# Performance work log

Measured on AMD Instinct MI355X. Metric: run time of the kernel, lower is better.

## Reference

```python
import jax, jax.numpy as jnp
import numpy as np

N_NODES = 100000
N_EDGES = 1600000
DIM = 64
L = 5
NUM_GRAPHS = 256
BN_EPS = 1e-5


def setup_inputs() -> dict:
    key = jax.random.key(0)
    ks = jax.random.split(key, 8)
    x = jax.random.normal(ks[0], (N_NODES, DIM), dtype=jnp.float32)
    edge_index = jax.random.randint(ks[1], (2, N_EDGES), 0, N_NODES, dtype=jnp.int32).astype(jnp.int64)
    batch = jnp.sort(jax.random.randint(ks[2], (N_NODES,), 0, NUM_GRAPHS, dtype=jnp.int32)).astype(jnp.int64)
    W1 = jax.random.normal(ks[3], (L, DIM, DIM), dtype=jnp.float32) * (1.0 / np.sqrt(DIM))
    b1 = jnp.zeros((L, DIM), dtype=jnp.float32)
    W2 = jax.random.normal(ks[4], (L, DIM, DIM), dtype=jnp.float32) * (1.0 / np.sqrt(DIM))
    b2 = jnp.zeros((L, DIM), dtype=jnp.float32)
    gamma = jnp.ones((L, DIM), dtype=jnp.float32)
    beta = jnp.zeros((L, DIM), dtype=jnp.float32)
    return {"x": x, "edge_index": edge_index, "batch": batch, "W1": W1, "b1": b1, "W2": W2, "b2": b2, "gamma": gamma, "beta": beta}


def reference(x, edge_index, batch, W1, b1, W2, b2, gamma, beta):
    src, dst = edge_index[0], edge_index[1]
    n = x.shape[0]
    h = x
    xs = []
    for i in range(L):
        # GINConv (eps=0): h_i' = MLP(h_i + sum_{j->i} h_j), scatter-add over edges
        agg = jax.ops.segment_sum(h[src], dst, num_segments=n)
        z = h + agg
        z = jnp.maximum(z @ W1[i] + b1[i], 0.0) @ W2[i] + b2[i]
        z = jnp.maximum(z, 0.0)  # outer ReLU
        # BatchNorm1d, training-mode batch stats (biased var)
        mu = jnp.mean(z, axis=0)
        var = jnp.mean((z - mu) ** 2, axis=0)
        z = (z - mu) * jax.lax.rsqrt(var + BN_EPS) * gamma[i] + beta[i]
        xs.append(z)
        h = z
    counts = jax.ops.segment_sum(jnp.ones((n,), dtype=x.dtype), batch, num_segments=NUM_GRAPHS)
    counts = jnp.maximum(counts, 1.0)[:, None]
    xpool = [jax.ops.segment_sum(z, batch, num_segments=NUM_GRAPHS) / counts for z in xs]
    return jnp.concatenate(xpool, axis=1), jnp.concatenate(xs, axis=1)
```

## Files before the change

kernel.cpp:

```cpp
#include <hip/hip_runtime.h>

#define N_NODES 100000
#define N_EDGES 1600000
#define DIM 64
#define NLAYERS 5
#define NUM_GRAPHS 256
#define BN_EPS 1e-5f
#define STATS_BLOCKS 256
#define CSR_CAP 32
#define OV_CAP 65536
#define NSHARD 4
#define SHARD_W (N_NODES / NSHARD)
#define NBLK ((N_NODES + 255) / 256)

typedef _Float16 f16;
typedef _Float16 f16x4 __attribute__((ext_vector_type(4)));

__global__ __launch_bounds__(256) void build_csr_shard_kernel(
        const int* __restrict__ ei, int* __restrict__ cursor,
        int* __restrict__ csr, int* __restrict__ ovcnt, int* __restrict__ ovpairs,
        int lo, int hi) {
    int e = blockIdx.x * 256 + threadIdx.x;
    if (e >= N_EDGES) return;
    int t = ei[N_EDGES + e];
    if (t < lo || t >= hi) return;
    int s = ei[e];
    int c = atomicAdd(&cursor[t], 1);
    if (c < CSR_CAP) {
        csr[t * CSR_CAP + c] = s;
    } else {
        int o = atomicAdd(ovcnt, 1);
        if (o < OV_CAP) { ovpairs[2 * o] = t; ovpairs[2 * o + 1] = s; }
    }
}

__global__ void cast_x_kernel(const float* __restrict__ x, f16* __restrict__ h16) {
    long t = (long)blockIdx.x * 256 + threadIdx.x;
    if (t >= (long)N_NODES * DIM / 4) return;
    float4 v = ((const float4*)x)[t];
    f16x4 p = { (f16)v.x, (f16)v.y, (f16)v.z, (f16)v.w };
    *(f16x4*)(h16 + t * 4) = p;
}

__global__ __launch_bounds__(256) void aggregate_f16_kernel(
        const int* __restrict__ csr, const int* __restrict__ deg,
        const int* __restrict__ ovcnt, const int* __restrict__ ovpairs,
        const f16* __restrict__ h16, const float* __restrict__ hself, int hstride,
        float* __restrict__ agg) {
    long tid = (long)blockIdx.x * 256 + threadIdx.x;
    int n = (int)(tid >> 6);
    int d = (int)(tid & 63);
    if (n >= N_NODES) return;
    int dval = deg[n];
    int cnt = min(dval, CSR_CAP);
    const int4* row = (const int4*)(csr + n * CSR_CAP);
    float own = hself[(long)n * hstride + d];
    float a0 = 0.f, a1 = 0.f, a2 = 0.f, a3 = 0.f;
    float a4 = 0.f, a5 = 0.f, a6 = 0.f, a7 = 0.f;
    for (int k = 0; k < cnt; k += 8) {
        int4 ra = row[k >> 2];
        int4 rb = row[(k >> 2) + 1];
        int s0 = (k + 0 < cnt) ? ra.x : 0;
        int s1 = (k + 1 < cnt) ? ra.y : 0;
        int s2 = (k + 2 < cnt) ? ra.z : 0;
        int s3 = (k + 3 < cnt) ? ra.w : 0;
        int s4 = (k + 4 < cnt) ? rb.x : 0;
        int s5 = (k + 5 < cnt) ? rb.y : 0;
        int s6 = (k + 6 < cnt) ? rb.z : 0;
        int s7 = (k + 7 < cnt) ? rb.w : 0;
        float v0 = (float)h16[(long)s0 * DIM + d];
        float v1 = (float)h16[(long)s1 * DIM + d];
        float v2 = (float)h16[(long)s2 * DIM + d];
        float v3 = (float)h16[(long)s3 * DIM + d];
        float v4 = (float)h16[(long)s4 * DIM + d];
        float v5 = (float)h16[(long)s5 * DIM + d];
        float v6 = (float)h16[(long)s6 * DIM + d];
        float v7 = (float)h16[(long)s7 * DIM + d];
        a0 += (k + 0 < cnt) ? v0 : 0.f;
        a1 += (k + 1 < cnt) ? v1 : 0.f;
        a2 += (k + 2 < cnt) ? v2 : 0.f;
        a3 += (k + 3 < cnt) ? v3 : 0.f;
        a4 += (k + 4 < cnt) ? v4 : 0.f;
        a5 += (k + 5 < cnt) ? v5 : 0.f;
        a6 += (k + 6 < cnt) ? v6 : 0.f;
        a7 += (k + 7 < cnt) ? v7 : 0.f;
    }
    if (dval > CSR_CAP) {
        int m = min(*ovcnt, OV_CAP);
        for (int i = 0; i < m; ++i) {
            if (ovpairs[2 * i] == n) a0 += (float)h16[(long)ovpairs[2 * i + 1] * DIM + d];
        }
    }
    agg[(long)n * DIM + d] = own + ((a0 + a1) + (a2 + a3)) + ((a4 + a5) + (a6 + a7));
}

__global__ __launch_bounds__(256) void mlp_gemm_kernel(
        const float* __restrict__ in, const float* __restrict__ W,
        const float* __restrict__ b, float* __restrict__ out) {
    __shared__ __align__(16) float sW[DIM * DIM];
    __shared__ float sb[DIM];
    for (int k = threadIdx.x; k < DIM * DIM / 4; k += 256)
        ((float4*)sW)[k] = ((const float4*)W)[k];
    if (threadIdx.x < DIM) sb[threadIdx.x] = b[threadIdx.x];
    __syncthreads();

    int p = threadIdx.x & 127;
    int j0 = (threadIdx.x >> 7) * 32;
    int base = blockIdx.x * 256;
    int n0 = base + p;
    int n1 = base + 128 + p;
    bool v1 = n1 < N_NODES;
    const float* inr0 = in + (long)n0 * DIM;
    const float* inr1 = in + (long)(v1 ? n1 : n0) * DIM;

    float acc0[32], acc1[32];
#pragma unroll
    for (int j = 0; j < 32; ++j) { acc0[j] = sb[j0 + j]; acc1[j] = acc0[j]; }

    for (int d4 = 0; d4 < DIM / 4; ++d4) {
        float4 za = ((const float4*)inr0)[d4];
        float4 zb = ((const float4*)inr1)[d4];
        const float* w0 = sW + (d4 * 4 + 0) * DIM + j0;
        const float* w1 = sW + (d4 * 4 + 1) * DIM + j0;
        const float* w2 = sW + (d4 * 4 + 2) * DIM + j0;
        const float* w3 = sW + (d4 * 4 + 3) * DIM + j0;
#pragma unroll
        for (int j = 0; j < 32; j += 4) {
            float4 a0 = *(const float4*)(w0 + j);
            float4 a1 = *(const float4*)(w1 + j);
            float4 a2 = *(const float4*)(w2 + j);
            float4 a3 = *(const float4*)(w3 + j);
            acc0[j + 0] += za.x * a0.x + za.y * a1.x + za.z * a2.x + za.w * a3.x;
            acc0[j + 1] += za.x * a0.y + za.y * a1.y + za.z * a2.y + za.w * a3.y;
            acc0[j + 2] += za.x * a0.z + za.y * a1.z + za.z * a2.z + za.w * a3.z;
            acc0[j + 3] += za.x * a0.w + za.y * a1.w + za.z * a2.w + za.w * a3.w;
            acc1[j + 0] += zb.x * a0.x + zb.y * a1.x + zb.z * a2.x + zb.w * a3.x;
            acc1[j + 1] += zb.x * a0.y + zb.y * a1.y + zb.z * a2.y + zb.w * a3.y;
            acc1[j + 2] += zb.x * a0.z + zb.y * a1.z + zb.z * a2.z + zb.w * a3.z;
            acc1[j + 3] += zb.x * a0.w + zb.y * a1.w + zb.z * a2.w + zb.w * a3.w;
        }
    }

    float* o0 = out + (long)n0 * DIM + j0;
#pragma unroll
    for (int j = 0; j < 32; j += 4) {
        float4 v = { fmaxf(acc0[j], 0.f), fmaxf(acc0[j + 1], 0.f),
                     fmaxf(acc0[j + 2], 0.f), fmaxf(acc0[j + 3], 0.f) };
        *(float4*)(o0 + j) = v;
    }
    if (v1) {
        float* o1 = out + (long)n1 * DIM + j0;
#pragma unroll
        for (int j = 0; j < 32; j += 4) {
            float4 v = { fmaxf(acc1[j], 0.f), fmaxf(acc1[j + 1], 0.f),
                         fmaxf(acc1[j + 2], 0.f), fmaxf(acc1[j + 3], 0.f) };
            *(float4*)(o1 + j) = v;
        }
    }
}

__global__ void stats_partial_kernel(const float* __restrict__ z, float* __restrict__ partials) {
    __shared__ float red[2 * 256];
    int d = threadIdx.x & 63;
    int slot = threadIdx.x >> 6;
    const int S = STATS_BLOCKS * 4;
    float s1 = 0.f, s2 = 0.f;
    int n = blockIdx.x * 4 + slot;
    for (; n + 3 * S < N_NODES; n += 4 * S) {
        float v0 = z[(long)(n + 0 * S) * DIM + d];
        float v1 = z[(long)(n + 1 * S) * DIM + d];
        float v2 = z[(long)(n + 2 * S) * DIM + d];
        float v3 = z[(long)(n + 3 * S) * DIM + d];
        s1 += v0 + v1 + v2 + v3;
        s2 += v0 * v0 + v1 * v1 + v2 * v2 + v3 * v3;
    }
    for (; n < N_NODES; n += S) {
        float v = z[(long)n * DIM + d];
        s1 += v;
        s2 += v * v;
    }
    red[threadIdx.x] = s1;
    red[256 + threadIdx.x] = s2;
    __syncthreads();
    if (threadIdx.x < 64) {
        float a = red[d] + red[64 + d] + red[128 + d] + red[192 + d];
        float c = red[256 + d] + red[320 + d] + red[384 + d] + red[448 + d];
        partials[blockIdx.x * 128 + d] = a;
        partials[blockIdx.x * 128 + 64 + d] = c;
    }
}

__global__ void stats_finalize_kernel(const float* __restrict__ partials,
                                      const float* __restrict__ gamma,
                                      const float* __restrict__ beta,
                                      float* __restrict__ ss) {
    __shared__ float r1[256], r2[256];
    int d = threadIdx.x & 63, q = threadIdx.x >> 6;
    float s1 = 0.f, s2 = 0.f;
    for (int b2_ = q; b2_ < STATS_BLOCKS; b2_ += 4) {
        s1 += partials[b2_ * 128 + d];
        s2 += partials[b2_ * 128 + 64 + d];
    }
    r1[threadIdx.x] = s1;
    r2[threadIdx.x] = s2;
    __syncthreads();
    if (threadIdx.x < 64) {
        s1 = r1[d] + r1[64 + d] + r1[128 + d] + r1[192 + d];
        s2 = r2[d] + r2[64 + d] + r2[128 + d] + r2[192 + d];
        float mu = s1 * (1.f / N_NODES);
        float var = s2 * (1.f / N_NODES) - mu * mu;
        float rs = 1.f / sqrtf(fmaxf(var, 0.f) + BN_EPS);
        float sc = gamma[d] * rs;
        ss[d] = sc;
        ss[64 + d] = beta[d] - mu * sc;
    }
}

__global__ void bn_apply_kernel(const float* __restrict__ z, const float* __restrict__ ss,
                                float* __restrict__ outxs, f16* __restrict__ h16) {
    long t = (long)blockIdx.x * 256 + threadIdx.x;
    if (t >= (long)N_NODES * (DIM / 4)) return;
    int r = (int)(t & 15);
    long n = t >> 4;
    float4 v = ((const float4*)(z + n * DIM))[r];
    float4 sc = ((const float4*)ss)[r];
    float4 sh = ((const float4*)(ss + DIM))[r];
    float4 o = { v.x * sc.x + sh.x, v.y * sc.y + sh.y,
                 v.z * sc.z + sh.z, v.w * sc.w + sh.w };
    ((float4*)(outxs + n * (DIM * NLAYERS)))[r] = o;
    if (h16) {
        f16x4 p = { (f16)o.x, (f16)o.y, (f16)o.z, (f16)o.w };
        *(f16x4*)(h16 + n * DIM + r * 4) = p;
    }
}

__global__ void graph_starts_kernel(const int* __restrict__ batch, int* __restrict__ starts) {
    int g = threadIdx.x;
    if (g > NUM_GRAPHS) return;
    int lo = 0, hi = N_NODES;
    while (lo < hi) {
        int mid = (lo + hi) >> 1;
        if (batch[mid] < g) lo = mid + 1; else hi = mid;
    }
    starts[g] = lo;
}

__global__ __launch_bounds__(64) void pool_kernel(
        const float* __restrict__ xs, const int* __restrict__ starts,
        float* __restrict__ outpool) {
    int g = blockIdx.x;
    int d = blockIdx.y * 64 + threadIdx.x;
    int s = starts[g], e = starts[g + 1];
    const int LD = DIM * NLAYERS;
    float a0 = 0.f, a1 = 0.f, a2 = 0.f, a3 = 0.f;
    float a4 = 0.f, a5 = 0.f, a6 = 0.f, a7 = 0.f;
    int n = s;
    for (; n + 8 <= e; n += 8) {
        a0 += xs[(long)(n + 0) * LD + d];
        a1 += xs[(long)(n + 1) * LD + d];
        a2 += xs[(long)(n + 2) * LD + d];
        a3 += xs[(long)(n + 3) * LD + d];
        a4 += xs[(long)(n + 4) * LD + d];
        a5 += xs[(long)(n + 5) * LD + d];
        a6 += xs[(long)(n + 6) * LD + d];
        a7 += xs[(long)(n + 7) * LD + d];
    }
    for (; n < e; ++n) a0 += xs[(long)n * LD + d];
    float acc = ((a0 + a1) + (a2 + a3)) + ((a4 + a5) + (a6 + a7));
    outpool[(long)g * LD + d] = acc / fmaxf((float)(e - s), 1.f);
}

static inline size_t rup(size_t x) { return (x + 255) & ~(size_t)255; }

extern "C" void kernel_launch(void* const* d_in, const int* in_sizes, int n_in,
                              void* d_out, int out_size, void* d_ws, size_t ws_size,
                              hipStream_t stream) {
    const float* x     = (const float*)d_in[0];
    const int*   ei    = (const int*)d_in[1];
    const int*   batch = (const int*)d_in[2];
    const float* W1    = (const float*)d_in[3];
    const float* b1    = (const float*)d_in[4];
    const float* W2    = (const float*)d_in[5];
    const float* b2    = (const float*)d_in[6];
    const float* gamma = (const float*)d_in[7];
    const float* beta  = (const float*)d_in[8];

    float* out      = (float*)d_out;
    float* out_pool = out;
    float* out_xs   = out + (size_t)NUM_GRAPHS * DIM * NLAYERS;

    char* w = (char*)d_ws;
    int*   csr      = (int*)w;    w += rup((size_t)N_NODES * CSR_CAP * 4);
    int*   cursor   = (int*)w;    w += rup((size_t)N_NODES * 4);
    int*   ovcnt    = (int*)w;    w += 256;
    int*   ovpairs  = (int*)w;    w += rup((size_t)OV_CAP * 8);
    float* agg      = (float*)w;  w += rup((size_t)N_NODES * DIM * 4);
    float* bufB     = (float*)w;  w += rup((size_t)N_NODES * DIM * 4);
    f16*   h16      = (f16*)w;    w += rup((size_t)N_NODES * DIM * 2);
    float* partials = (float*)w;  w += rup((size_t)STATS_BLOCKS * 128 * 4);
    float* ss       = (float*)w;  w += 512;
    int*   starts   = (int*)w;    w += rup((size_t)(NUM_GRAPHS + 1) * 4);
    float* zbuf     = agg;

    hipMemsetAsync(cursor, 0, (size_t)N_NODES * 4, stream);
    hipMemsetAsync(ovcnt, 0, 4, stream);
    for (int sh = 0; sh < NSHARD; ++sh) {
        build_csr_shard_kernel<<<(N_EDGES + 255) / 256, 256, 0, stream>>>(
            ei, cursor, csr, ovcnt, ovpairs, sh * SHARD_W, (sh + 1) * SHARD_W);
    }
    cast_x_kernel<<<((long)N_NODES * DIM / 4 + 255) / 256, 256, 0, stream>>>(x, h16);
    graph_starts_kernel<<<1, 320, 0, stream>>>(batch, starts);

    const float* hself = x;
    int hs = DIM;
    for (int l = 0; l < NLAYERS; ++l) {
        aggregate_f16_kernel<<<((long)N_NODES * DIM + 255) / 256, 256, 0, stream>>>(
            csr, cursor, ovcnt, ovpairs, h16, hself, hs, agg);
        mlp_gemm_kernel<<<NBLK, 256, 0, stream>>>(
            agg, W1 + (size_t)l * DIM * DIM, b1 + (size_t)l * DIM, bufB);
        mlp_gemm_kernel<<<NBLK, 256, 0, stream>>>(
            bufB, W2 + (size_t)l * DIM * DIM, b2 + (size_t)l * DIM, zbuf);
        stats_partial_kernel<<<STATS_BLOCKS, 256, 0, stream>>>(zbuf, partials);
        stats_finalize_kernel<<<1, 256, 0, stream>>>(partials, gamma + (size_t)l * DIM,
                                                     beta + (size_t)l * DIM, ss);
        bn_apply_kernel<<<((long)N_NODES * (DIM / 4) + 255) / 256, 256, 0, stream>>>(
            zbuf, ss, out_xs + (size_t)l * DIM, (l + 1 < NLAYERS) ? h16 : nullptr);
        hself = out_xs + (size_t)l * DIM;
        hs = DIM * NLAYERS;
    }

    pool_kernel<<<dim3(NUM_GRAPHS, NLAYERS), 64, 0, stream>>>(out_xs, starts, out_pool);
}
```

Baseline: 863.1 us.

## Vectorize aggregation to half2 per lane and fuse BN stats finalize via last-block

The aggregation kernel now gives each half-wavefront one node, and each lane loads two fp16 features (f16x2) per neighbor. This halves the number of gather instructions and widens the stores to float2. The separate stats finalize launch is folded into the partial-stats kernel using a last-block-done atomic counter stored next to ovcnt. This saves one launch per layer but adds a threadfence and an atomic handshake.

```diff
diff --git a/kernel.cpp b/kernel.cpp
--- a/kernel.cpp
+++ b/kernel.cpp
@@ -14,6 +14,7 @@
 #define NBLK ((N_NODES + 255) / 256)
 
 typedef _Float16 f16;
+typedef _Float16 f16x2 __attribute__((ext_vector_type(2)));
 typedef _Float16 f16x4 __attribute__((ext_vector_type(4)));
 
 __global__ __launch_bounds__(256) void build_csr_shard_kernel(
@@ -47,19 +48,24 @@
         const int* __restrict__ ovcnt, const int* __restrict__ ovpairs,
         const f16* __restrict__ h16, const float* __restrict__ hself, int hstride,
         float* __restrict__ agg) {
-    long tid = (long)blockIdx.x * 256 + threadIdx.x;
-    int n = (int)(tid >> 6);
-    int d = (int)(tid & 63);
-    if (n >= N_NODES) return;
+    int lane = threadIdx.x & 63;
+    int half = lane >> 5;
+    int ll = lane & 31;
+    int n = blockIdx.x * 8 + (threadIdx.x >> 6) * 2 + half;
+
     int dval = deg[n];
     int cnt = min(dval, CSR_CAP);
-    const int4* row = (const int4*)(csr + n * CSR_CAP);
-    float own = hself[(long)n * hstride + d];
-    float a0 = 0.f, a1 = 0.f, a2 = 0.f, a3 = 0.f;
-    float a4 = 0.f, a5 = 0.f, a6 = 0.f, a7 = 0.f;
+    const int4* row4 = (const int4*)(csr + n * CSR_CAP);
+
+    float2 own = *(const float2*)(hself + (long)n * hstride + 2 * ll);
+    float ax0 = own.x, ay0 = own.y;
+    float ax1 = 0.f, ay1 = 0.f, ax2 = 0.f, ay2 = 0.f, ax3 = 0.f, ay3 = 0.f;
+    float ax4 = 0.f, ay4 = 0.f, ax5 = 0.f, ay5 = 0.f, ax6 = 0.f, ay6 = 0.f;
+    float ax7 = 0.f, ay7 = 0.f;
+
     for (int k = 0; k < cnt; k += 8) {
-        int4 ra = row[k >> 2];
-        int4 rb = row[(k >> 2) + 1];
+        int4 ra = row4[k >> 2];
+        int4 rb = row4[(k >> 2) + 1];
         int s0 = (k + 0 < cnt) ? ra.x : 0;
         int s1 = (k + 1 < cnt) ? ra.y : 0;
         int s2 = (k + 2 < cnt) ? ra.z : 0;
@@ -68,30 +74,35 @@
         int s5 = (k + 5 < cnt) ? rb.y : 0;
         int s6 = (k + 6 < cnt) ? rb.z : 0;
         int s7 = (k + 7 < cnt) ? rb.w : 0;
-        float v0 = (float)h16[(long)s0 * DIM + d];
-        float v1 = (float)h16[(long)s1 * DIM + d];
-        float v2 = (float)h16[(long)s2 * DIM + d];
-        float v3 = (float)h16[(long)s3 * DIM + d];
-        float v4 = (float)h16[(long)s4 * DIM + d];
-        float v5 = (float)h16[(long)s5 * DIM + d];
-        float v6 = (float)h16[(long)s6 * DIM + d];
-        float v7 = (float)h16[(long)s7 * DIM + d];
-        a0 += (k + 0 < cnt) ? v0 : 0.f;
-        a1 += (k + 1 < cnt) ? v1 : 0.f;
-        a2 += (k + 2 < cnt) ? v2 : 0.f;
-        a3 += (k + 3 < cnt) ? v3 : 0.f;
-        a4 += (k + 4 < cnt) ? v4 : 0.f;
-        a5 += (k + 5 < cnt) ? v5 : 0.f;
-        a6 += (k + 6 < cnt) ? v6 : 0.f;
-        a7 += (k + 7 < cnt) ? v7 : 0.f;
+        f16x2 v0 = *(const f16x2*)(h16 + (long)s0 * DIM + 2 * ll);
+        f16x2 v1 = *(const f16x2*)(h16 + (long)s1 * DIM + 2 * ll);
+        f16x2 v2 = *(const f16x2*)(h16 + (long)s2 * DIM + 2 * ll);
+        f16x2 v3 = *(const f16x2*)(h16 + (long)s3 * DIM + 2 * ll);
+        f16x2 v4 = *(const f16x2*)(h16 + (long)s4 * DIM + 2 * ll);
+        f16x2 v5 = *(const f16x2*)(h16 + (long)s5 * DIM + 2 * ll);
+        f16x2 v6 = *(const f16x2*)(h16 + (long)s6 * DIM + 2 * ll);
+        f16x2 v7 = *(const f16x2*)(h16 + (long)s7 * DIM + 2 * ll);
+        if (k + 0 < cnt) { ax0 += (float)v0.x; ay0 += (float)v0.y; }
+        if (k + 1 < cnt) { ax1 += (float)v1.x; ay1 += (float)v1.y; }
+        if (k + 2 < cnt) { ax2 += (float)v2.x; ay2 += (float)v2.y; }
+        if (k + 3 < cnt) { ax3 += (float)v3.x; ay3 += (float)v3.y; }
+        if (k + 4 < cnt) { ax4 += (float)v4.x; ay4 += (float)v4.y; }
+        if (k + 5 < cnt) { ax5 += (float)v5.x; ay5 += (float)v5.y; }
+        if (k + 6 < cnt) { ax6 += (float)v6.x; ay6 += (float)v6.y; }
+        if (k + 7 < cnt) { ax7 += (float)v7.x; ay7 += (float)v7.y; }
     }
     if (dval > CSR_CAP) {
         int m = min(*ovcnt, OV_CAP);
         for (int i = 0; i < m; ++i) {
-            if (ovpairs[2 * i] == n) a0 += (float)h16[(long)ovpairs[2 * i + 1] * DIM + d];
+            if (ovpairs[2 * i] == n) {
+                f16x2 v = *(const f16x2*)(h16 + (long)ovpairs[2 * i + 1] * DIM + 2 * ll);
+                ax0 += (float)v.x; ay0 += (float)v.y;
+            }
         }
     }
-    agg[(long)n * DIM + d] = own + ((a0 + a1) + (a2 + a3)) + ((a4 + a5) + (a6 + a7));
+    float2 o = { ((ax0 + ax1) + (ax2 + ax3)) + ((ax4 + ax5) + (ax6 + ax7)),
+                 ((ay0 + ay1) + (ay2 + ay3)) + ((ay4 + ay5) + (ay6 + ay7)) };
+    *(float2*)(agg + (long)n * DIM + 2 * ll) = o;
 }
 
 __global__ __launch_bounds__(256) void mlp_gemm_kernel(
@@ -159,8 +170,13 @@
     }
 }
 
-__global__ void stats_partial_kernel(const float* __restrict__ z, float* __restrict__ partials) {
+__global__ void stats_kernel(const float* __restrict__ z,
+                             const float* __restrict__ gamma,
+                             const float* __restrict__ beta,
+                             float* __restrict__ partials, float* __restrict__ ss,
+                             int* __restrict__ done) {
     __shared__ float red[2 * 256];
+    __shared__ int lastflag;
     int d = threadIdx.x & 63;
     int slot = threadIdx.x >> 6;
     const int S = STATS_BLOCKS * 4;
@@ -188,32 +204,37 @@
         partials[blockIdx.x * 128 + d] = a;
         partials[blockIdx.x * 128 + 64 + d] = c;
     }
-}
-
-__global__ void stats_finalize_kernel(const float* __restrict__ partials,
-                                      const float* __restrict__ gamma,
-                                      const float* __restrict__ beta,
-                                      float* __restrict__ ss) {
-    __shared__ float r1[256], r2[256];
-    int d = threadIdx.x & 63, q = threadIdx.x >> 6;
-    float s1 = 0.f, s2 = 0.f;
-    for (int b2_ = q; b2_ < STATS_BLOCKS; b2_ += 4) {
-        s1 += partials[b2_ * 128 + d];
-        s2 += partials[b2_ * 128 + 64 + d];
-    }
-    r1[threadIdx.x] = s1;
-    r2[threadIdx.x] = s2;
+    __threadfence();
+    __syncthreads();
+    if (threadIdx.x == 0)
+        lastflag = (atomicAdd(done, 1) == STATS_BLOCKS - 1);
+    __syncthreads();
+    if (!lastflag) return;
+
+    int q = threadIdx.x >> 6;
+    float t1 = 0.f, t2 = 0.f;
+    for (int b = q; b < STATS_BLOCKS; b += 4) {
+        t1 += __hip_atomic_load(&partials[b * 128 + d], __ATOMIC_RELAXED,
+                                __HIP_MEMORY_SCOPE_AGENT);
+        t2 += __hip_atomic_load(&partials[b * 128 + 64 + d], __ATOMIC_RELAXED,
+                                __HIP_MEMORY_SCOPE_AGENT);
+    }
+    __syncthreads();
+    red[threadIdx.x] = t1;
+    red[256 + threadIdx.x] = t2;
     __syncthreads();
     if (threadIdx.x < 64) {
-        s1 = r1[d] + r1[64 + d] + r1[128 + d] + r1[192 + d];
-        s2 = r2[d] + r2[64 + d] + r2[128 + d] + r2[192 + d];
-        float mu = s1 * (1.f / N_NODES);
-        float var = s2 * (1.f / N_NODES) - mu * mu;
+        t1 = red[d] + red[64 + d] + red[128 + d] + red[192 + d];
+        t2 = red[256 + d] + red[320 + d] + red[384 + d] + red[448 + d];
+        float mu = t1 * (1.f / N_NODES);
+        float var = t2 * (1.f / N_NODES) - mu * mu;
         float rs = 1.f / sqrtf(fmaxf(var, 0.f) + BN_EPS);
         float sc = gamma[d] * rs;
         ss[d] = sc;
         ss[64 + d] = beta[d] - mu * sc;
     }
+    if (threadIdx.x == 0)
+        __hip_atomic_store(done, 0, __ATOMIC_RELAXED, __HIP_MEMORY_SCOPE_AGENT);
 }
 
 __global__ void bn_apply_kernel(const float* __restrict__ z, const float* __restrict__ ss,
@@ -303,7 +324,7 @@
     float* zbuf     = agg;
 
     hipMemsetAsync(cursor, 0, (size_t)N_NODES * 4, stream);
-    hipMemsetAsync(ovcnt, 0, 4, stream);
+    hipMemsetAsync(ovcnt, 0, 8, stream);
     for (int sh = 0; sh < NSHARD; ++sh) {
         build_csr_shard_kernel<<<(N_EDGES + 255) / 256, 256, 0, stream>>>(
             ei, cursor, csr, ovcnt, ovpairs, sh * SHARD_W, (sh + 1) * SHARD_W);
@@ -314,15 +335,15 @@
     const float* hself = x;
     int hs = DIM;
     for (int l = 0; l < NLAYERS; ++l) {
-        aggregate_f16_kernel<<<((long)N_NODES * DIM + 255) / 256, 256, 0, stream>>>(
+        aggregate_f16_kernel<<<N_NODES / 8, 256, 0, stream>>>(
             csr, cursor, ovcnt, ovpairs, h16, hself, hs, agg);
         mlp_gemm_kernel<<<NBLK, 256, 0, stream>>>(
             agg, W1 + (size_t)l * DIM * DIM, b1 + (size_t)l * DIM, bufB);
         mlp_gemm_kernel<<<NBLK, 256, 0, stream>>>(
             bufB, W2 + (size_t)l * DIM * DIM, b2 + (size_t)l * DIM, zbuf);
-        stats_partial_kernel<<<STATS_BLOCKS, 256, 0, stream>>>(zbuf, partials);
-        stats_finalize_kernel<<<1, 256, 0, stream>>>(partials, gamma + (size_t)l * DIM,
-                                                     beta + (size_t)l * DIM, ss);
+        stats_kernel<<<STATS_BLOCKS, 256, 0, stream>>>(
+            zbuf, gamma + (size_t)l * DIM, beta + (size_t)l * DIM,
+            partials, ss, ovcnt + 1);
         bn_apply_kernel<<<((long)N_NODES * (DIM / 4) + 255) / 256, 256, 0, stream>>>(
             zbuf, ss, out_xs + (size_t)l * DIM, (l + 1 < NLAYERS) ? h16 : nullptr);
         hself = out_xs + (size_t)l * DIM;
```

Result: slower. 906.6 us (+5.0%).

## Retile MLP GEMM to four rows per thread and fuse BN stats finalize

Applied to the files above, without the earlier changes.

The MLP GEMM now has each thread compute 4 node rows by 16 output columns instead of 2 rows by 32 columns. Each weight value read from shared memory is therefore reused across more rows. Separately, the BN statistics finalize step moves into the partial-stats kernel using a last-block-done atomic counter, which removes one kernel launch per layer. The counter lives next to the overflow count and relies on __threadfence plus relaxed atomic loads for correctness.

```diff
diff --git a/kernel.cpp b/kernel.cpp
--- a/kernel.cpp
+++ b/kernel.cpp
@@ -104,63 +104,79 @@
     if (threadIdx.x < DIM) sb[threadIdx.x] = b[threadIdx.x];
     __syncthreads();
 
-    int p = threadIdx.x & 127;
-    int j0 = (threadIdx.x >> 7) * 32;
+    int p = threadIdx.x & 63;
+    int j0 = (threadIdx.x >> 6) * 16;
     int base = blockIdx.x * 256;
     int n0 = base + p;
-    int n1 = base + 128 + p;
-    bool v1 = n1 < N_NODES;
-    const float* inr0 = in + (long)n0 * DIM;
-    const float* inr1 = in + (long)(v1 ? n1 : n0) * DIM;
-
-    float acc0[32], acc1[32];
+    int n1 = base + 64 + p;
+    int n2 = base + 128 + p;
+    int n3 = base + 192 + p;
+    int c0 = min(n0, N_NODES - 1), c1 = min(n1, N_NODES - 1);
+    int c2 = min(n2, N_NODES - 1), c3 = min(n3, N_NODES - 1);
+    const float* i0 = in + (long)c0 * DIM;
+    const float* i1 = in + (long)c1 * DIM;
+    const float* i2 = in + (long)c2 * DIM;
+    const float* i3 = in + (long)c3 * DIM;
+
+    float acc0[16], acc1[16], acc2[16], acc3[16];
 #pragma unroll
-    for (int j = 0; j < 32; ++j) { acc0[j] = sb[j0 + j]; acc1[j] = acc0[j]; }
+    for (int j = 0; j < 16; ++j) {
+        float bv = sb[j0 + j];
+        acc0[j] = bv; acc1[j] = bv; acc2[j] = bv; acc3[j] = bv;
+    }
 
     for (int d4 = 0; d4 < DIM / 4; ++d4) {
-        float4 za = ((const float4*)inr0)[d4];
-        float4 zb = ((const float4*)inr1)[d4];
+        float4 z0 = ((const float4*)i0)[d4];
+        float4 z1 = ((const float4*)i1)[d4];
+        float4 z2 = ((const float4*)i2)[d4];
+        float4 z3 = ((const float4*)i3)[d4];
         const float* w0 = sW + (d4 * 4 + 0) * DIM + j0;
         const float* w1 = sW + (d4 * 4 + 1) * DIM + j0;
         const float* w2 = sW + (d4 * 4 + 2) * DIM + j0;
         const float* w3 = sW + (d4 * 4 + 3) * DIM + j0;
 #pragma unroll
-        for (int j = 0; j < 32; j += 4) {
+        for (int j = 0; j < 16; j += 4) {
             float4 a0 = *(const float4*)(w0 + j);
             float4 a1 = *(const float4*)(w1 + j);
             float4 a2 = *(const float4*)(w2 + j);
             float4 a3 = *(const float4*)(w3 + j);
-            acc0[j + 0] += za.x * a0.x + za.y * a1.x + za.z * a2.x + za.w * a3.x;
-            acc0[j + 1] += za.x * a0.y + za.y * a1.y + za.z * a2.y + za.w * a3.y;
-            acc0[j + 2] += za.x * a0.z + za.y * a1.z + za.z * a2.z + za.w * a3.z;
-            acc0[j + 3] += za.x * a0.w + za.y * a1.w + za.z * a2.w + za.w * a3.w;
-            acc1[j + 0] += zb.x * a0.x + zb.y * a1.x + zb.z * a2.x + zb.w * a3.x;
-            acc1[j + 1] += zb.x * a0.y + zb.y * a1.y + zb.z * a2.y + zb.w * a3.y;
-            acc1[j + 2] += zb.x * a0.z + zb.y * a1.z + zb.z * a2.z + zb.w * a3.z;
-            acc1[j + 3] += zb.x * a0.w + zb.y * a1.w + zb.z * a2.w + zb.w * a3.w;
+#define GEMM_ONE(ACC, Z)                                                    \
+            ACC[j + 0] += Z.x * a0.x + Z.y * a1.x + Z.z * a2.x + Z.w * a3.x; \
+            ACC[j + 1] += Z.x * a0.y + Z.y * a1.y + Z.z * a2.y + Z.w * a3.y; \
+            ACC[j + 2] += Z.x * a0.z + Z.y * a1.z + Z.z * a2.z + Z.w * a3.z; \
+            ACC[j + 3] += Z.x * a0.w + Z.y * a1.w + Z.z * a2.w + Z.w * a3.w;
+            GEMM_ONE(acc0, z0)
+            GEMM_ONE(acc1, z1)
+            GEMM_ONE(acc2, z2)
+            GEMM_ONE(acc3, z3)
+#undef GEMM_ONE
         }
     }
 
-    float* o0 = out + (long)n0 * DIM + j0;
-#pragma unroll
-    for (int j = 0; j < 32; j += 4) {
-        float4 v = { fmaxf(acc0[j], 0.f), fmaxf(acc0[j + 1], 0.f),
-                     fmaxf(acc0[j + 2], 0.f), fmaxf(acc0[j + 3], 0.f) };
-        *(float4*)(o0 + j) = v;
-    }
-    if (v1) {
-        float* o1 = out + (long)n1 * DIM + j0;
-#pragma unroll
-        for (int j = 0; j < 32; j += 4) {
-            float4 v = { fmaxf(acc1[j], 0.f), fmaxf(acc1[j + 1], 0.f),
-                         fmaxf(acc1[j + 2], 0.f), fmaxf(acc1[j + 3], 0.f) };
-            *(float4*)(o1 + j) = v;
-        }
-    }
-}
-
-__global__ void stats_partial_kernel(const float* __restrict__ z, float* __restrict__ partials) {
+#define STORE_ONE(N, ACC)                                                   \
+    if (N < N_NODES) {                                                      \
+        float* o = out + (long)N * DIM + j0;                                \
+        _Pragma("unroll")                                                   \
+        for (int j = 0; j < 16; j += 4) {                                   \
+            float4 v = { fmaxf(ACC[j], 0.f), fmaxf(ACC[j + 1], 0.f),        \
+                         fmaxf(ACC[j + 2], 0.f), fmaxf(ACC[j + 3], 0.f) };  \
+            *(float4*)(o + j) = v;                                          \
+        }                                                                   \
+    }
+    STORE_ONE(n0, acc0)
+    STORE_ONE(n1, acc1)
+    STORE_ONE(n2, acc2)
+    STORE_ONE(n3, acc3)
+#undef STORE_ONE
+}
+
+__global__ void stats_kernel(const float* __restrict__ z,
+                             const float* __restrict__ gamma,
+                             const float* __restrict__ beta,
+                             float* __restrict__ partials, float* __restrict__ ss,
+                             int* __restrict__ done) {
     __shared__ float red[2 * 256];
+    __shared__ int lastflag;
     int d = threadIdx.x & 63;
     int slot = threadIdx.x >> 6;
     const int S = STATS_BLOCKS * 4;
@@ -188,32 +204,37 @@
         partials[blockIdx.x * 128 + d] = a;
         partials[blockIdx.x * 128 + 64 + d] = c;
     }
-}
-
-__global__ void stats_finalize_kernel(const float* __restrict__ partials,
-                                      const float* __restrict__ gamma,
-                                      const float* __restrict__ beta,
-                                      float* __restrict__ ss) {
-    __shared__ float r1[256], r2[256];
-    int d = threadIdx.x & 63, q = threadIdx.x >> 6;
-    float s1 = 0.f, s2 = 0.f;
-    for (int b2_ = q; b2_ < STATS_BLOCKS; b2_ += 4) {
-        s1 += partials[b2_ * 128 + d];
-        s2 += partials[b2_ * 128 + 64 + d];
-    }
-    r1[threadIdx.x] = s1;
-    r2[threadIdx.x] = s2;
+    __threadfence();
+    __syncthreads();
+    if (threadIdx.x == 0)
+        lastflag = (atomicAdd(done, 1) == STATS_BLOCKS - 1);
+    __syncthreads();
+    if (!lastflag) return;
+
+    int q = threadIdx.x >> 6;
+    float t1 = 0.f, t2 = 0.f;
+    for (int b = q; b < STATS_BLOCKS; b += 4) {
+        t1 += __hip_atomic_load(&partials[b * 128 + d], __ATOMIC_RELAXED,
+                                __HIP_MEMORY_SCOPE_AGENT);
+        t2 += __hip_atomic_load(&partials[b * 128 + 64 + d], __ATOMIC_RELAXED,
+                                __HIP_MEMORY_SCOPE_AGENT);
+    }
+    __syncthreads();
+    red[threadIdx.x] = t1;
+    red[256 + threadIdx.x] = t2;
     __syncthreads();
     if (threadIdx.x < 64) {
-        s1 = r1[d] + r1[64 + d] + r1[128 + d] + r1[192 + d];
-        s2 = r2[d] + r2[64 + d] + r2[128 + d] + r2[192 + d];
-        float mu = s1 * (1.f / N_NODES);
-        float var = s2 * (1.f / N_NODES) - mu * mu;
+        t1 = red[d] + red[64 + d] + red[128 + d] + red[192 + d];
+        t2 = red[256 + d] + red[320 + d] + red[384 + d] + red[448 + d];
+        float mu = t1 * (1.f / N_NODES);
+        float var = t2 * (1.f / N_NODES) - mu * mu;
         float rs = 1.f / sqrtf(fmaxf(var, 0.f) + BN_EPS);
         float sc = gamma[d] * rs;
         ss[d] = sc;
         ss[64 + d] = beta[d] - mu * sc;
     }
+    if (threadIdx.x == 0)
+        __hip_atomic_store(done, 0, __ATOMIC_RELAXED, __HIP_MEMORY_SCOPE_AGENT);
 }
 
 __global__ void bn_apply_kernel(const float* __restrict__ z, const float* __restrict__ ss,
@@ -303,7 +324,7 @@
     float* zbuf     = agg;
 
     hipMemsetAsync(cursor, 0, (size_t)N_NODES * 4, stream);
-    hipMemsetAsync(ovcnt, 0, 4, stream);
+    hipMemsetAsync(ovcnt, 0, 8, stream);
     for (int sh = 0; sh < NSHARD; ++sh) {
         build_csr_shard_kernel<<<(N_EDGES + 255) / 256, 256, 0, stream>>>(
             ei, cursor, csr, ovcnt, ovpairs, sh * SHARD_W, (sh + 1) * SHARD_W);
@@ -320,9 +341,9 @@
             agg, W1 + (size_t)l * DIM * DIM, b1 + (size_t)l * DIM, bufB);
         mlp_gemm_kernel<<<NBLK, 256, 0, stream>>>(
             bufB, W2 + (size_t)l * DIM * DIM, b2 + (size_t)l * DIM, zbuf);
-        stats_partial_kernel<<<STATS_BLOCKS, 256, 0, stream>>>(zbuf, partials);
-        stats_finalize_kernel<<<1, 256, 0, stream>>>(partials, gamma + (size_t)l * DIM,
-                                                     beta + (size_t)l * DIM, ss);
+        stats_kernel<<<STATS_BLOCKS, 256, 0, stream>>>(
+            zbuf, gamma + (size_t)l * DIM, beta + (size_t)l * DIM,
+            partials, ss, ovcnt + 1);
         bn_apply_kernel<<<((long)N_NODES * (DIM / 4) + 255) / 256, 256, 0, stream>>>(
             zbuf, ss, out_xs + (size_t)l * DIM, (l + 1 < NLAYERS) ? h16 : nullptr);
         hself = out_xs + (size_t)l * DIM;
```

Result: slower. 946.8 us (+9.7%).
